# Kernel tuning notes

Measured on AMD Instinct MI355X. Metric: run time of the kernel, lower is better.

## Reference

```python
import jax, jax.numpy as jnp
import numpy as np

L, B, T, D, H, M = 2, 4, 1024, 256, 4, 1024
EPS = 1e-5  # hk.LayerNorm default


def setup_inputs() -> dict:
    key = jax.random.key(0)
    ks = jax.random.split(key, 12)
    s_in = (2.0 / D) ** 0.5       # VarianceScaling(2.0), fan_in = D
    s_o = (2.0 / (H * D)) ** 0.5  # fan_in = H*D for final projection
    s_m = (1.0 / M) ** 0.5
    g = lambda k, shape, s: jax.random.normal(k, shape, jnp.float32) * s
    return {
        "queries": g(ks[0], (B, T, D), 1.0),
        "Wq": g(ks[1], (L, D, H * D), s_in),
        "bq": jnp.zeros((L, H * D), jnp.float32),
        "Wk": g(ks[2], (L, D, H * D), s_in),
        "bk": jnp.zeros((L, H * D), jnp.float32),
        "Wv": g(ks[3], (L, D, H * D), s_in),
        "bv": jnp.zeros((L, H * D), jnp.float32),
        "Wo": g(ks[4], (L, H * D, D), s_o),
        "bo": jnp.zeros((L, D), jnp.float32),
        "ln1_s": jnp.ones((L, D), jnp.float32),
        "ln1_b": jnp.zeros((L, D), jnp.float32),
        "W1": g(ks[5], (L, D, M), s_in),
        "b1": jnp.zeros((L, M), jnp.float32),
        "W2": g(ks[6], (L, M, D), s_m),
        "b2": jnp.zeros((L, D), jnp.float32),
        "ln2_s": jnp.ones((L, D), jnp.float32),
        "ln2_b": jnp.zeros((L, D), jnp.float32),
    }


def _layernorm(x, s, o):
    m = jnp.mean(x, axis=-1, keepdims=True)
    v = jnp.var(x, axis=-1, keepdims=True)
    return (x - m) * jax.lax.rsqrt(v + EPS) * s + o


def _block(x, Wq, bq, Wk, bk, Wv, bv, Wo, bo, ln1_s, ln1_b, W1, b1, W2, b2, ln2_s, ln2_b):
    # Multi-head self-attention with per-head dim = D (key_size == qkv_size)
    q = (x @ Wq + bq).reshape(B, T, H, D)
    k = (x @ Wk + bk).reshape(B, T, H, D)
    v = (x @ Wv + bv).reshape(B, T, H, D)
    q = q / jnp.sqrt(jnp.float32(D))
    attn = jnp.einsum('bqhd,bkhd->bhqk', q, k)   # [B,H,T,T]
    attn = jax.nn.softmax(attn, axis=-1)
    o = jnp.einsum('bhqk,bkhd->bqhd', attn, v).reshape(B, T, H * D)
    o = o @ Wo + bo
    # post-norm residual 1
    x = _layernorm(o + x, ln1_s, ln1_b)
    # MLP: Linear(D->M) + ReLU + Linear(M->D)
    h = jax.nn.relu(x @ W1 + b1)
    m = h @ W2 + b2
    return _layernorm(m + x, ln2_s, ln2_b)


def reference(queries, Wq, bq, Wk, bk, Wv, bv, Wo, bo, ln1_s, ln1_b,
              W1, b1, W2, b2, ln2_s, ln2_b):
    x = queries
    for i in range(L):
        x = _block(x, Wq[i], bq[i], Wk[i], bk[i], Wv[i], bv[i], Wo[i], bo[i],
                   ln1_s[i], ln1_b[i], W1[i], b1[i], W2[i], b2[i],
                   ln2_s[i], ln2_b[i])
    return x
```

## Files before the change

kernel.cpp:

```cpp
#include <hip/hip_runtime.h>
#include <hip/hip_bf16.h>

#define CL 2
#define CB 4
#define CT 1024
#define CD 256
#define CH 4
#define CM 1024
#define CHD (CH * CD)
#define NROW (CB * CT)

typedef unsigned short ushort_t;
typedef __attribute__((ext_vector_type(8))) short short8v;
typedef __attribute__((ext_vector_type(4))) float float4v;

#define LOG2E 1.44269504088896f

__device__ __forceinline__ float bf2f(unsigned short u) {
    return __uint_as_float(((unsigned int)u) << 16);
}
__device__ __forceinline__ unsigned short f2bf(float f) {
    unsigned int x = __float_as_uint(f);
    return (unsigned short)((x + 0x7fffu + ((x >> 16) & 1u)) >> 16);
}

__global__ __launch_bounds__(256) void detect_kernel(
    const ushort_t* __restrict__ w, int n, int* __restrict__ flag)
{
    __shared__ int red[256];
    int c = 0;
    for (int i = threadIdx.x; i < n; i += 256) {
        float v = bf2f(w[i]);
        if (!(fabsf(v) <= 1e6f)) c++;
    }
    red[threadIdx.x] = c;
    __syncthreads();
    for (int s = 128; s > 0; s >>= 1) {
        if (threadIdx.x < s) red[threadIdx.x] += red[threadIdx.x + s];
        __syncthreads();
    }
    if (threadIdx.x == 0) flag[0] = (red[0] < 8) ? 1 : 0;
}

__global__ __launch_bounds__(256) void tconv_all(
    const void* __restrict__ Wq, const void* __restrict__ Wk,
    const void* __restrict__ Wv, const void* __restrict__ W1,
    ushort_t* __restrict__ wqkvT, ushort_t* __restrict__ w1T,
    const int* __restrict__ flagp)
{
    const int fbf = *flagp;
    const int z = blockIdx.z;
    const int which = z >> 1, l = z & 1;
    const void* in = (which == 0) ? Wq : (which == 1) ? Wk
                   : (which == 2) ? Wv : W1;
    ushort_t* out = (which < 3)
        ? wqkvT + (long)l * 3072 * 256 + (long)which * 1024 * 256
        : w1T + (long)l * 1024 * 256;
    const long zi = (long)l * 262144;

    __shared__ float tile[32][33];
    const int r0 = blockIdx.y * 32;
    const int c0 = blockIdx.x * 32;
    const int tx = threadIdx.x & 31;
    const int ty = threadIdx.x >> 5;
#pragma unroll
    for (int i = 0; i < 32; i += 8) {
        const long idx = zi + (long)(r0 + ty + i) * 1024 + c0 + tx;
        tile[ty + i][tx] = fbf ? bf2f(((const ushort_t*)in)[idx])
                               : ((const float*)in)[idx];
    }
    __syncthreads();
#pragma unroll
    for (int i = 0; i < 32; i += 8)
        out[(long)(c0 + ty + i) * 256 + r0 + tx] = f2bf(tile[tx][ty + i]);
}

__global__ __launch_bounds__(256) void tconv2(
    const void* __restrict__ Wo, const void* __restrict__ W2,
    ushort_t* __restrict__ wscr, long ioff, const int* __restrict__ flagp)
{
    const int fbf = *flagp;
    const int z = blockIdx.z;
    const void* in = z ? W2 : Wo;
    ushort_t* out = wscr + (long)z * 262144;

    __shared__ float tile[32][33];
    const int r0 = blockIdx.y * 32;
    const int c0 = blockIdx.x * 32;
    const int tx = threadIdx.x & 31;
    const int ty = threadIdx.x >> 5;
#pragma unroll
    for (int i = 0; i < 32; i += 8) {
        const long idx = ioff + (long)(r0 + ty + i) * 256 + c0 + tx;
        tile[ty + i][tx] = fbf ? bf2f(((const ushort_t*)in)[idx])
                               : ((const float*)in)[idx];
    }
    __syncthreads();
#pragma unroll
    for (int i = 0; i < 32; i += 8)
        out[(long)(c0 + ty + i) * 1024 + r0 + tx] = f2bf(tile[tx][ty + i]);
}

__global__ __launch_bounds__(256) void qkv_proj(
    const ushort_t* __restrict__ A, const ushort_t* __restrict__ B,
    const void* __restrict__ bq, const void* __restrict__ bk,
    const void* __restrict__ bv, ushort_t* __restrict__ qk,
    ushort_t* __restrict__ vT, long boff, const int* __restrict__ flagp)
{
    const long m0 = (long)blockIdx.y * 128;
    const long n0 = (long)blockIdx.x * 128;

    __shared__ __align__(16) ushort_t As[128 * 40];
    __shared__ __align__(16) ushort_t Bs[128 * 40];

    const int tid = threadIdx.x;
    const int wave = tid >> 6;
    const int lane = tid & 63;
    const int quad = lane >> 4;
    const int lrow = lane & 15;
    const int wm = (wave >> 1) * 64;
    const int wn = (wave & 1) * 64;

    float4v acc[4][4];
#pragma unroll
    for (int i = 0; i < 4; ++i)
#pragma unroll
        for (int j = 0; j < 4; ++j)
            acc[i][j] = (float4v){0.f, 0.f, 0.f, 0.f};

    for (int k0 = 0; k0 < 256; k0 += 32) {
        __syncthreads();
#pragma unroll
        for (int p = 0; p < 2; ++p) {
            const int c = p * 256 + tid;
            const int row = c >> 2;
            const int kk = (c & 3) << 3;
            *reinterpret_cast<short8v*>(&As[row * 40 + kk]) =
                *reinterpret_cast<const short8v*>(&A[(m0 + row) * 256 + k0 + kk]);
            *reinterpret_cast<short8v*>(&Bs[row * 40 + kk]) =
                *reinterpret_cast<const short8v*>(&B[(n0 + row) * 256 + k0 + kk]);
        }
        __syncthreads();

        short8v af[4], bfv[4];
#pragma unroll
        for (int i = 0; i < 4; ++i) {
            af[i]  = *reinterpret_cast<const short8v*>(&As[(wm + i * 16 + lrow) * 40 + quad * 8]);
            bfv[i] = *reinterpret_cast<const short8v*>(&Bs[(wn + i * 16 + lrow) * 40 + quad * 8]);
        }
#pragma unroll
        for (int mi = 0; mi < 4; ++mi)
#pragma unroll
            for (int ni = 0; ni < 4; ++ni)
                acc[mi][ni] = __builtin_amdgcn_mfma_f32_16x16x32_bf16(
                    af[mi], bfv[ni], acc[mi][ni], 0, 0, 0);
    }

    const int fbf = *flagp;
#pragma unroll
    for (int mi = 0; mi < 4; ++mi) {
#pragma unroll
        for (int ni = 0; ni < 4; ++ni) {
            const long col = n0 + wn + ni * 16 + lrow;
            const long row0 = m0 + wm + mi * 16 + quad * 4;
            const void* bp;
            long bn;
            if (col < 1024)      { bp = bq; bn = col; }
            else if (col < 2048) { bp = bk; bn = col - 1024; }
            else                 { bp = bv; bn = col - 2048; }
            const float bias = fbf ? bf2f(((const ushort_t*)bp)[boff + bn])
                                   : ((const float*)bp)[boff + bn];
            if (col < 2048) {
#pragma unroll
                for (int r = 0; r < 4; ++r)
                    qk[(row0 + r) * 2048 + col] = f2bf(acc[mi][ni][r] + bias);
            } else {
                const long d = col - 2048;
                const long addr = ((row0 >> 10) << 2) * 262144 + d * 1024 + (row0 & 1023);
                ushort4 u;
                u.x = f2bf(acc[mi][ni][0] + bias);
                u.y = f2bf(acc[mi][ni][1] + bias);
                u.z = f2bf(acc[mi][ni][2] + bias);
                u.w = f2bf(acc[mi][ni][3] + bias);
                *reinterpret_cast<ushort4*>(&vT[addr]) = u;
            }
        }
    }
}

template <int AMODE>
__global__ __launch_bounds__(256) void mgemm64s(
    const ushort_t* __restrict__ A, const ushort_t* __restrict__ Ap1,
    const float2* __restrict__ ml, const ushort_t* __restrict__ B,
    float* __restrict__ P, int K2, int lda, int ldb)
{
    const int z = blockIdx.z;
    const long m0 = (long)blockIdx.y * 64;
    const long n0 = (long)blockIdx.x * 64;
    const int k_beg = z * K2;

    __shared__ __align__(16) ushort_t As[64 * 40];
    __shared__ __align__(16) ushort_t Bs[64 * 40];

    const int tid = threadIdx.x;
    const int wave = tid >> 6;
    const int lane = tid & 63;
    const int quad = lane >> 4;
    const int lrow = lane & 15;
    const int wm = (wave >> 1) * 32;
    const int wn = (wave & 1) * 32;

    const int ar = tid >> 2;
    const int ak = (tid & 3) << 3;

    float4v acc[2][2];
#pragma unroll
    for (int i = 0; i < 2; ++i)
#pragma unroll
        for (int j = 0; j < 2; ++j)
            acc[i][j] = (float4v){0.f, 0.f, 0.f, 0.f};

    for (int k0 = k_beg; k0 < k_beg + K2; k0 += 32) {
        __syncthreads();
        if constexpr (AMODE == 0) {
            *reinterpret_cast<short8v*>(&As[ar * 40 + ak]) =
                *reinterpret_cast<const short8v*>(&A[(m0 + ar) * (long)lda + k0 + ak]);
        } else {
            const long m = m0 + ar;
            const int hh = (k0 + ak) >> 8;
            const int bh = ((int)(m >> 10) << 2) + hh;
            const int trow = (int)(m & 1023);
            const float2 v0 = ml[bh * 1024 + trow];
            const float2 v1 = ml[(16 + bh) * 1024 + trow];
            const float mm = fmaxf(v0.x, v1.x);
            const float a0 = exp2f(v0.x - mm);
            const float a1 = exp2f(v1.x - mm);
            const float inv = 1.0f / (v0.y * a0 + v1.y * a1);
            const ushort4 u0a = *reinterpret_cast<const ushort4*>(&A[m * 1024 + k0 + ak]);
            const ushort4 u0b = *reinterpret_cast<const ushort4*>(&A[m * 1024 + k0 + ak + 4]);
            const ushort4 u1a = *reinterpret_cast<const ushort4*>(&Ap1[m * 1024 + k0 + ak]);
            const ushort4 u1b = *reinterpret_cast<const ushort4*>(&Ap1[m * 1024 + k0 + ak + 4]);
            short8v t8;
            t8[0] = (short)f2bf((bf2f(u0a.x) * a0 + bf2f(u1a.x) * a1) * inv);
            t8[1] = (short)f2bf((bf2f(u0a.y) * a0 + bf2f(u1a.y) * a1) * inv);
            t8[2] = (short)f2bf((bf2f(u0a.z) * a0 + bf2f(u1a.z) * a1) * inv);
            t8[3] = (short)f2bf((bf2f(u0a.w) * a0 + bf2f(u1a.w) * a1) * inv);
            t8[4] = (short)f2bf((bf2f(u0b.x) * a0 + bf2f(u1b.x) * a1) * inv);
            t8[5] = (short)f2bf((bf2f(u0b.y) * a0 + bf2f(u1b.y) * a1) * inv);
            t8[6] = (short)f2bf((bf2f(u0b.z) * a0 + bf2f(u1b.z) * a1) * inv);
            t8[7] = (short)f2bf((bf2f(u0b.w) * a0 + bf2f(u1b.w) * a1) * inv);
            *reinterpret_cast<short8v*>(&As[ar * 40 + ak]) = t8;
        }
        *reinterpret_cast<short8v*>(&Bs[ar * 40 + ak]) =
            *reinterpret_cast<const short8v*>(&B[(n0 + ar) * (long)ldb + k0 + ak]);
        __syncthreads();

        short8v af[2], bfv[2];
#pragma unroll
        for (int i = 0; i < 2; ++i) {
            af[i]  = *reinterpret_cast<const short8v*>(&As[(wm + i * 16 + lrow) * 40 + quad * 8]);
            bfv[i] = *reinterpret_cast<const short8v*>(&Bs[(wn + i * 16 + lrow) * 40 + quad * 8]);
        }
#pragma unroll
        for (int mi = 0; mi < 2; ++mi)
#pragma unroll
            for (int ni = 0; ni < 2; ++ni)
                acc[mi][ni] = __builtin_amdgcn_mfma_f32_16x16x32_bf16(
                    af[mi], bfv[ni], acc[mi][ni], 0, 0, 0);
    }

    float* Pz = P + (long)z * NROW * CD;
#pragma unroll
    for (int mi = 0; mi < 2; ++mi)
#pragma unroll
        for (int ni = 0; ni < 2; ++ni) {
            const long col = n0 + wn + ni * 16 + lrow;
            const long row0 = m0 + wm + mi * 16 + quad * 4;
#pragma unroll
            for (int r = 0; r < 4; ++r)
                Pz[(row0 + r) * CD + col] = acc[mi][ni][r];
        }
}

template <int RELU>
__global__ __launch_bounds__(256) void mgemm64b(
    const ushort_t* __restrict__ A, const ushort_t* __restrict__ B,
    const void* __restrict__ bias, ushort_t* __restrict__ C,
    int K, int lda, int ldb, int ldc, long boff,
    const int* __restrict__ flagp)
{
    const long m0 = (long)blockIdx.y * 64;
    const long n0 = (long)blockIdx.x * 64;

    __shared__ __align__(16) ushort_t As[64 * 40];
    __shared__ __align__(16) ushort_t Bs[64 * 40];

    const int tid = threadIdx.x;
    const int wave = tid >> 6;
    const int lane = tid & 63;
    const int quad = lane >> 4;
    const int lrow = lane & 15;
    const int wm = (wave >> 1) * 32;
    const int wn = (wave & 1) * 32;

    const int ar = tid >> 2;
    const int ak = (tid & 3) << 3;

    float4v acc[2][2];
#pragma unroll
    for (int i = 0; i < 2; ++i)
#pragma unroll
        for (int j = 0; j < 2; ++j)
            acc[i][j] = (float4v){0.f, 0.f, 0.f, 0.f};

    for (int k0 = 0; k0 < K; k0 += 32) {
        __syncthreads();
        *reinterpret_cast<short8v*>(&As[ar * 40 + ak]) =
            *reinterpret_cast<const short8v*>(&A[(m0 + ar) * (long)lda + k0 + ak]);
        *reinterpret_cast<short8v*>(&Bs[ar * 40 + ak]) =
            *reinterpret_cast<const short8v*>(&B[(n0 + ar) * (long)ldb + k0 + ak]);
        __syncthreads();

        short8v af[2], bfv[2];
#pragma unroll
        for (int i = 0; i < 2; ++i) {
            af[i]  = *reinterpret_cast<const short8v*>(&As[(wm + i * 16 + lrow) * 40 + quad * 8]);
            bfv[i] = *reinterpret_cast<const short8v*>(&Bs[(wn + i * 16 + lrow) * 40 + quad * 8]);
        }
#pragma unroll
        for (int mi = 0; mi < 2; ++mi)
#pragma unroll
            for (int ni = 0; ni < 2; ++ni)
                acc[mi][ni] = __builtin_amdgcn_mfma_f32_16x16x32_bf16(
                    af[mi], bfv[ni], acc[mi][ni], 0, 0, 0);
    }

    const int fbf = *flagp;
#pragma unroll
    for (int mi = 0; mi < 2; ++mi)
#pragma unroll
        for (int ni = 0; ni < 2; ++ni) {
            const long col = n0 + wn + ni * 16 + lrow;
            const long row0 = m0 + wm + mi * 16 + quad * 4;
            const float bv = fbf ? bf2f(((const ushort_t*)bias)[boff + col])
                                 : ((const float*)bias)[boff + col];
#pragma unroll
            for (int r = 0; r < 4; ++r) {
                float v = acc[mi][ni][r] + bv;
                if (RELU) v = fmaxf(v, 0.f);
                C[(row0 + r) * (long)ldc + col] = f2bf(v);
            }
        }
}

__global__ __launch_bounds__(256) void flash_attn(
    const ushort_t* __restrict__ qk, const ushort_t* __restrict__ vT,
    ushort_t* __restrict__ op0, ushort_t* __restrict__ op1,
    float2* __restrict__ ml)
{
    const int bx = blockIdx.x;
    const int bh = bx & 15;
    const int qt = (bx >> 4) & 15;
    const int ck = bx >> 8;
    const int b = bh >> 2, h = bh & 3;

    __shared__ __align__(16) ushort_t Ks[32 * 264];
    __shared__ __align__(16) ushort_t Vs[256 * 40];
    __shared__ __align__(16) ushort_t Ps[4][16 * 40];

    const int tid = threadIdx.x;
    const int wave = tid >> 6;
    const int lane = tid & 63;
    const int quad = lane >> 4;
    const int lrow = lane & 15;

    const long qrow0 = (long)b * CT + qt * 64;
    const int qcol = h * 256;
    const int kcol = 1024 + h * 256;
    const long vbase = (long)bh * 256 * 1024;
    const float SC = 0.0625f * LOG2E;

    short8v qf[8];
#pragma unroll
    for (int kk = 0; kk < 8; ++kk)
        qf[kk] = *reinterpret_cast<const short8v*>(
            &qk[(qrow0 + wave * 16 + lrow) * 2048 + qcol + kk * 32 + quad * 8]);

    float mrun = -1e30f, lrun = 0.f;
    float4v oacc[16];
#pragma unroll
    for (int i = 0; i < 16; ++i) oacc[i] = (float4v){0.f, 0.f, 0.f, 0.f};

    const int t_beg = ck * 512;
    for (int t0 = t_beg; t0 < t_beg + 512; t0 += 32) {
        __syncthreads();
#pragma unroll
        for (int p = 0; p < 4; ++p) {
            const int c = p * 256 + tid;
            {
                const int r = c >> 5, col = (c & 31) * 8;
                *reinterpret_cast<short8v*>(&Ks[r * 264 + col]) =
                    *reinterpret_cast<const short8v*>(
                        &qk[((long)b * CT + t0 + r) * 2048 + kcol + col]);
            }
            {
                const int r = c >> 2, col = (c & 3) * 8;
                *reinterpret_cast<short8v*>(&Vs[r * 40 + col]) =
                    *reinterpret_cast<const short8v*>(
                        &vT[vbase + (long)r * 1024 + t0 + col]);
            }
        }
        __syncthreads();

        float4v sacc[2];
        sacc[0] = (float4v){0.f, 0.f, 0.f, 0.f};
        sacc[1] = (float4v){0.f, 0.f, 0.f, 0.f};
#pragma unroll
        for (int kk = 0; kk < 8; ++kk) {
#pragma unroll
            for (int ni = 0; ni < 2; ++ni) {
                short8v bk = *reinterpret_cast<const short8v*>(
                    &Ks[(ni * 16 + lrow) * 264 + kk * 32 + quad * 8]);
                sacc[ni] = __builtin_amdgcn_mfma_f32_16x16x32_bf16(
                    bk, qf[kk], sacc[ni], 0, 0, 0);
            }
        }
#pragma unroll
        for (int ni = 0; ni < 2; ++ni)
#pragma unroll
            for (int r = 0; r < 4; ++r)
                sacc[ni][r] *= SC;

        float mx = fmaxf(fmaxf(fmaxf(sacc[0][0], sacc[0][1]),
                               fmaxf(sacc[0][2], sacc[0][3])),
                         fmaxf(fmaxf(sacc[1][0], sacc[1][1]),
                               fmaxf(sacc[1][2], sacc[1][3])));
        mx = fmaxf(mx, __shfl_xor(mx, 16));
        mx = fmaxf(mx, __shfl_xor(mx, 32));

        if (__ballot(mx > mrun + 1.0f) != 0ull) {
            const float mnew = fmaxf(mrun, mx);
            const float alpha = exp2f(mrun - mnew);
            mrun = mnew;
            lrun *= alpha;
            float a4[4];
#pragma unroll
            for (int r = 0; r < 4; ++r)
                a4[r] = __shfl(alpha, quad * 4 + r);
#pragma unroll
            for (int ni = 0; ni < 16; ++ni)
#pragma unroll
                for (int r = 0; r < 4; ++r)
                    oacc[ni][r] *= a4[r];
        }

        float s = 0.f;
#pragma unroll
        for (int ni = 0; ni < 2; ++ni) {
            ushort4 pu;
#pragma unroll
            for (int r = 0; r < 4; ++r) {
                const float pv = exp2f(sacc[ni][r] - mrun);
                s += pv;
                (&pu.x)[r] = f2bf(pv);
            }
            *reinterpret_cast<ushort4*>(
                &Ps[wave][lrow * 40 + ni * 16 + quad * 4]) = pu;
        }
        s += __shfl_xor(s, 16);
        s += __shfl_xor(s, 32);
        lrun += s;

        {
            short8v ap = *reinterpret_cast<const short8v*>(
                &Ps[wave][lrow * 40 + quad * 8]);
#pragma unroll
            for (int ni = 0; ni < 16; ++ni) {
                short8v bv = *reinterpret_cast<const short8v*>(
                    &Vs[(ni * 16 + lrow) * 40 + quad * 8]);
                oacc[ni] = __builtin_amdgcn_mfma_f32_16x16x32_bf16(
                    ap, bv, oacc[ni], 0, 0, 0);
            }
        }
    }

    if (quad == 0)
        ml[((ck << 4) + bh) * 1024 + qt * 64 + wave * 16 + lrow] =
            make_float2(mrun, lrun);

    ushort_t* op = ck ? op1 : op0;
#pragma unroll
    for (int ni = 0; ni < 16; ++ni)
#pragma unroll
        for (int r = 0; r < 4; ++r)
            op[(qrow0 + wave * 16 + quad * 4 + r) * 1024 + (h << 8) + ni * 16 + lrow]
                = f2bf(oacc[ni][r]);
}

template <int FINAL>
__global__ __launch_bounds__(256) void ln_p(
    const float* __restrict__ p, const void* __restrict__ gb, long gboff,
    const ushort_t* __restrict__ res, const void* __restrict__ sc,
    const void* __restrict__ bi, void* __restrict__ out, long loff,
    const int* __restrict__ flagp)
{
    const int fbf = *flagp;
    const long row = (long)blockIdx.x * CD;
    const int t = threadIdx.x;
    const float gbv = fbf ? bf2f(((const ushort_t*)gb)[gboff + t])
                          : ((const float*)gb)[gboff + t];
    const float x = p[row + t] + p[(long)NROW * CD + row + t] + gbv + bf2f(res[row + t]);

    __shared__ float r1[256];
    __shared__ float r2[256];
    r1[t] = x;
    r2[t] = x * x;
    __syncthreads();
    for (int s = 128; s > 0; s >>= 1) {
        if (t < s) { r1[t] += r1[t + s]; r2[t] += r2[t + s]; }
        __syncthreads();
    }
    const float mean = r1[0] * (1.0f / CD);
    const float var = r2[0] * (1.0f / CD) - mean * mean;
    const float rstd = rsqrtf(var + 1e-5f);
    const float s_v = fbf ? bf2f(((const ushort_t*)sc)[loff + t]) : ((const float*)sc)[loff + t];
    const float b_v = fbf ? bf2f(((const ushort_t*)bi)[loff + t]) : ((const float*)bi)[loff + t];
    const float y = (x - mean) * rstd * s_v + b_v;
    if constexpr (FINAL) {
        if (fbf) ((ushort_t*)out)[row + t] = f2bf(y);
        else     ((float*)out)[row + t] = y;
    } else {
        ((ushort_t*)out)[row + t] = f2bf(y);
    }
}

__global__ __launch_bounds__(256) void in_convert(
    const void* __restrict__ in, ushort_t* __restrict__ x,
    const int* __restrict__ flagp)
{
    const int fbf = *flagp;
    const long i = ((long)blockIdx.x * 256 + threadIdx.x) << 2;
    if (fbf) {
        *reinterpret_cast<ushort4*>(x + i) =
            *reinterpret_cast<const ushort4*>((const ushort_t*)in + i);
    } else {
        float4 f = *reinterpret_cast<const float4*>((const float*)in + i);
        ushort4 u;
        u.x = f2bf(f.x); u.y = f2bf(f.y); u.z = f2bf(f.z); u.w = f2bf(f.w);
        *reinterpret_cast<ushort4*>(x + i) = u;
    }
}

extern "C" void kernel_launch(void* const* d_in, const int* in_sizes, int n_in,
                              void* d_out, int out_size, void* d_ws, size_t ws_size,
                              hipStream_t stream)
{
    const void* queries = d_in[0];
    const void* Wq = d_in[1];  const void* bq = d_in[2];
    const void* Wk = d_in[3];  const void* bk = d_in[4];
    const void* Wv = d_in[5];  const void* bv = d_in[6];
    const void* Wo = d_in[7];  const void* bo = d_in[8];
    const void* ln1s = d_in[9];  const void* ln1b = d_in[10];
    const void* W1 = d_in[11]; const void* b1 = d_in[12];
    const void* W2 = d_in[13]; const void* b2 = d_in[14];
    const void* ln2s = d_in[15]; const void* ln2b = d_in[16];

    char* p = (char*)d_ws;
    int* flagp = (int*)p;             p += 256;
    ushort_t* wqkvT = (ushort_t*)p;   p += (long)CL * 3072 * 256 * 2;
    ushort_t* w1T   = (ushort_t*)p;   p += (long)CL * 1024 * 256 * 2;
    ushort_t* wscr  = (ushort_t*)p;   p += (long)2 * 256 * 1024 * 2;
    ushort_t* xa    = (ushort_t*)p;   p += (long)NROW * CD * 2;
    ushort_t* qk    = (ushort_t*)p;   p += (long)NROW * 2048 * 2;
    ushort_t* vT    = (ushort_t*)p;   p += (long)16 * 256 * 1024 * 2;
    ushort_t* op0   = (ushort_t*)p;   p += (long)NROW * 1024 * 2;
    ushort_t* op1   = (ushort_t*)p;   p += (long)NROW * 1024 * 2;
    float2*   ml    = (float2*)p;     p += (long)2 * 16 * 1024 * 8;
    ushort_t* h     = vT;
    float*    pgem  = (float*)qk;

    detect_kernel<<<1, 256, 0, stream>>>((const ushort_t*)Wq, 2048, flagp);
    tconv_all<<<dim3(32, 8, 8), 256, 0, stream>>>(
        Wq, Wk, Wv, W1, wqkvT, w1T, flagp);
    in_convert<<<(NROW * CD) / 1024, 256, 0, stream>>>(queries, xa, flagp);

    for (int l = 0; l < CL; ++l) {
        qkv_proj<<<dim3(24, 32, 1), 256, 0, stream>>>(
            xa, wqkvT + (long)l * 3072 * 256, bq, bk, bv, qk, vT,
            (long)l * 1024, flagp);
        tconv2<<<dim3(8, 32, 2), 256, 0, stream>>>(
            Wo, W2, wscr, (long)l * 1024 * 256, flagp);
        flash_attn<<<512, 256, 0, stream>>>(qk, vT, op0, op1, ml);
        mgemm64s<1><<<dim3(4, 64, 2), 256, 0, stream>>>(
            op0, op1, ml, wscr, pgem, 512, 1024, 1024);
        ln_p<0><<<NROW, 256, 0, stream>>>(pgem, bo, (long)l * 256, xa,
                                          ln1s, ln1b, xa, (long)l * 256, flagp);
        mgemm64b<1><<<dim3(16, 64, 1), 256, 0, stream>>>(
            xa, w1T + (long)l * 1024 * 256, b1, h,
            256, 256, 256, 1024, (long)l * 1024, flagp);
        mgemm64s<0><<<dim3(4, 64, 2), 256, 0, stream>>>(
            h, nullptr, nullptr, wscr + 262144, pgem, 512, 1024, 1024);
        if (l == CL - 1)
            ln_p<1><<<NROW, 256, 0, stream>>>(pgem, b2, (long)l * 256, xa,
                                              ln2s, ln2b, d_out, (long)l * 256, flagp);
        else
            ln_p<0><<<NROW, 256, 0, stream>>>(pgem, b2, (long)l * 256, xa,
                                              ln2s, ln2b, xa, (long)l * 256, flagp);
    }
}
```

Before: 322.4 us.

## Fuse Wo/W2 transpose into QKV projection launch and deepen GEMM K-tiles

The per-layer weight-transpose kernel is merged into the QKV projection kernel as extra blocks in a flat 1D grid (blocks at index 768 and above do the transpose), which removes one launch per layer. The small 64x64 GEMMs now stage 64-wide K chunks instead of 32, halving the number of barrier pairs per K loop at the cost of more LDS. The split-softmax combine in the attention-output GEMM now computes its per-head rescale factors once, before the K loop, instead of recomputing exp and divide on every iteration. The fused kernel carries the transpose tile in shared memory for every block, which raises LDS use and may lower occupancy.

```diff
diff --git a/kernel.cpp b/kernel.cpp
--- a/kernel.cpp
+++ b/kernel.cpp
@@ -75,45 +75,52 @@
         out[(long)(c0 + ty + i) * 256 + r0 + tx] = f2bf(tile[tx][ty + i]);
 }
 
-__global__ __launch_bounds__(256) void tconv2(
-    const void* __restrict__ Wo, const void* __restrict__ W2,
-    ushort_t* __restrict__ wscr, long ioff, const int* __restrict__ flagp)
-{
-    const int fbf = *flagp;
-    const int z = blockIdx.z;
-    const void* in = z ? W2 : Wo;
-    ushort_t* out = wscr + (long)z * 262144;
-
-    __shared__ float tile[32][33];
-    const int r0 = blockIdx.y * 32;
-    const int c0 = blockIdx.x * 32;
-    const int tx = threadIdx.x & 31;
-    const int ty = threadIdx.x >> 5;
-#pragma unroll
-    for (int i = 0; i < 32; i += 8) {
-        const long idx = ioff + (long)(r0 + ty + i) * 256 + c0 + tx;
-        tile[ty + i][tx] = fbf ? bf2f(((const ushort_t*)in)[idx])
-                               : ((const float*)in)[idx];
-    }
-    __syncthreads();
-#pragma unroll
-    for (int i = 0; i < 32; i += 8)
-        out[(long)(c0 + ty + i) * 1024 + r0 + tx] = f2bf(tile[tx][ty + i]);
-}
-
-__global__ __launch_bounds__(256) void qkv_proj(
+__global__ __launch_bounds__(256) void qkv_tconv(
     const ushort_t* __restrict__ A, const ushort_t* __restrict__ B,
     const void* __restrict__ bq, const void* __restrict__ bk,
     const void* __restrict__ bv, ushort_t* __restrict__ qk,
-    ushort_t* __restrict__ vT, long boff, const int* __restrict__ flagp)
-{
-    const long m0 = (long)blockIdx.y * 128;
-    const long n0 = (long)blockIdx.x * 128;
-
+    ushort_t* __restrict__ vT,
+    const void* __restrict__ Wo, const void* __restrict__ W2,
+    ushort_t* __restrict__ wscr,
+    long boff, long ioff, const int* __restrict__ flagp)
+{
     __shared__ __align__(16) ushort_t As[128 * 40];
     __shared__ __align__(16) ushort_t Bs[128 * 40];
-
+    __shared__ float tile[32][33];
+
+    const int fbf = *flagp;
+    const int bx = blockIdx.x;
     const int tid = threadIdx.x;
+
+    if (bx >= 768) {
+        const int t = bx - 768;
+        const int zx = t & 7;
+        const int zy = (t >> 3) & 31;
+        const int zz = t >> 8;
+        const void* in = zz ? W2 : Wo;
+        ushort_t* out = wscr + (long)zz * 262144;
+        const int r0 = zy * 32;
+        const int c0 = zx * 32;
+        const int tx = tid & 31;
+        const int ty = tid >> 5;
+#pragma unroll
+        for (int i = 0; i < 32; i += 8) {
+            const long idx = ioff + (long)(r0 + ty + i) * 256 + c0 + tx;
+            tile[ty + i][tx] = fbf ? bf2f(((const ushort_t*)in)[idx])
+                                   : ((const float*)in)[idx];
+        }
+        __syncthreads();
+#pragma unroll
+        for (int i = 0; i < 32; i += 8)
+            out[(long)(c0 + ty + i) * 1024 + r0 + tx] = f2bf(tile[tx][ty + i]);
+        return;
+    }
+
+    const int nt = bx % 24;
+    const int mt = bx / 24;
+    const long m0 = (long)mt * 128;
+    const long n0 = (long)nt * 128;
+
     const int wave = tid >> 6;
     const int lane = tid & 63;
     const int quad = lane >> 4;
@@ -156,7 +163,6 @@
                     af[mi], bfv[ni], acc[mi][ni], 0, 0, 0);
     }
 
-    const int fbf = *flagp;
 #pragma unroll
     for (int mi = 0; mi < 4; ++mi) {
 #pragma unroll
@@ -199,8 +205,8 @@
     const long n0 = (long)blockIdx.x * 64;
     const int k_beg = z * K2;
 
-    __shared__ __align__(16) ushort_t As[64 * 40];
-    __shared__ __align__(16) ushort_t Bs[64 * 40];
+    __shared__ __align__(16) ushort_t As[64 * 72];
+    __shared__ __align__(16) ushort_t Bs[64 * 72];
 
     const int tid = threadIdx.x;
     const int wave = tid >> 6;
@@ -213,60 +219,82 @@
     const int ar = tid >> 2;
     const int ak = (tid & 3) << 3;
 
-    float4v acc[2][2];
-#pragma unroll
-    for (int i = 0; i < 2; ++i)
-#pragma unroll
-        for (int j = 0; j < 2; ++j)
-            acc[i][j] = (float4v){0.f, 0.f, 0.f, 0.f};
-
-    for (int k0 = k_beg; k0 < k_beg + K2; k0 += 32) {
-        __syncthreads();
-        if constexpr (AMODE == 0) {
-            *reinterpret_cast<short8v*>(&As[ar * 40 + ak]) =
-                *reinterpret_cast<const short8v*>(&A[(m0 + ar) * (long)lda + k0 + ak]);
-        } else {
-            const long m = m0 + ar;
-            const int hh = (k0 + ak) >> 8;
-            const int bh = ((int)(m >> 10) << 2) + hh;
-            const int trow = (int)(m & 1023);
+    float s0h[2] = {0.f, 0.f}, s1h[2] = {0.f, 0.f};
+    if constexpr (AMODE == 1) {
+        const long m = m0 + ar;
+        const int bhbase = ((int)(m >> 10) << 2);
+        const int trow = (int)(m & 1023);
+        const int h0 = k_beg >> 8;
+#pragma unroll
+        for (int i = 0; i < 2; ++i) {
+            const int bh = bhbase + h0 + i;
             const float2 v0 = ml[bh * 1024 + trow];
             const float2 v1 = ml[(16 + bh) * 1024 + trow];
             const float mm = fmaxf(v0.x, v1.x);
             const float a0 = exp2f(v0.x - mm);
             const float a1 = exp2f(v1.x - mm);
             const float inv = 1.0f / (v0.y * a0 + v1.y * a1);
-            const ushort4 u0a = *reinterpret_cast<const ushort4*>(&A[m * 1024 + k0 + ak]);
-            const ushort4 u0b = *reinterpret_cast<const ushort4*>(&A[m * 1024 + k0 + ak + 4]);
-            const ushort4 u1a = *reinterpret_cast<const ushort4*>(&Ap1[m * 1024 + k0 + ak]);
-            const ushort4 u1b = *reinterpret_cast<const ushort4*>(&Ap1[m * 1024 + k0 + ak + 4]);
-            short8v t8;
-            t8[0] = (short)f2bf((bf2f(u0a.x) * a0 + bf2f(u1a.x) * a1) * inv);
-            t8[1] = (short)f2bf((bf2f(u0a.y) * a0 + bf2f(u1a.y) * a1) * inv);
-            t8[2] = (short)f2bf((bf2f(u0a.z) * a0 + bf2f(u1a.z) * a1) * inv);
-            t8[3] = (short)f2bf((bf2f(u0a.w) * a0 + bf2f(u1a.w) * a1) * inv);
-            t8[4] = (short)f2bf((bf2f(u0b.x) * a0 + bf2f(u1b.x) * a1) * inv);
-            t8[5] = (short)f2bf((bf2f(u0b.y) * a0 + bf2f(u1b.y) * a1) * inv);
-            t8[6] = (short)f2bf((bf2f(u0b.z) * a0 + bf2f(u1b.z) * a1) * inv);
-            t8[7] = (short)f2bf((bf2f(u0b.w) * a0 + bf2f(u1b.w) * a1) * inv);
-            *reinterpret_cast<short8v*>(&As[ar * 40 + ak]) = t8;
-        }
-        *reinterpret_cast<short8v*>(&Bs[ar * 40 + ak]) =
-            *reinterpret_cast<const short8v*>(&B[(n0 + ar) * (long)ldb + k0 + ak]);
-        __syncthreads();
-
-        short8v af[2], bfv[2];
-#pragma unroll
-        for (int i = 0; i < 2; ++i) {
-            af[i]  = *reinterpret_cast<const short8v*>(&As[(wm + i * 16 + lrow) * 40 + quad * 8]);
-            bfv[i] = *reinterpret_cast<const short8v*>(&Bs[(wn + i * 16 + lrow) * 40 + quad * 8]);
-        }
-#pragma unroll
-        for (int mi = 0; mi < 2; ++mi)
-#pragma unroll
-            for (int ni = 0; ni < 2; ++ni)
-                acc[mi][ni] = __builtin_amdgcn_mfma_f32_16x16x32_bf16(
-                    af[mi], bfv[ni], acc[mi][ni], 0, 0, 0);
+            s0h[i] = a0 * inv;
+            s1h[i] = a1 * inv;
+        }
+    }
+
+    float4v acc[2][2];
+#pragma unroll
+    for (int i = 0; i < 2; ++i)
+#pragma unroll
+        for (int j = 0; j < 2; ++j)
+            acc[i][j] = (float4v){0.f, 0.f, 0.f, 0.f};
+
+    for (int k0 = k_beg; k0 < k_beg + K2; k0 += 64) {
+        __syncthreads();
+#pragma unroll
+        for (int p = 0; p < 2; ++p) {
+            const int kc = p * 32 + ak;
+            if constexpr (AMODE == 0) {
+                *reinterpret_cast<short8v*>(&As[ar * 72 + kc]) =
+                    *reinterpret_cast<const short8v*>(&A[(m0 + ar) * (long)lda + k0 + kc]);
+            } else {
+                const long m = m0 + ar;
+                const int hi = ((k0 + kc) >> 8) - (k_beg >> 8);
+                const float s0 = s0h[hi], s1 = s1h[hi];
+                const ushort4 u0a = *reinterpret_cast<const ushort4*>(&A[m * 1024 + k0 + kc]);
+                const ushort4 u0b = *reinterpret_cast<const ushort4*>(&A[m * 1024 + k0 + kc + 4]);
+                const ushort4 u1a = *reinterpret_cast<const ushort4*>(&Ap1[m * 1024 + k0 + kc]);
+                const ushort4 u1b = *reinterpret_cast<const ushort4*>(&Ap1[m * 1024 + k0 + kc + 4]);
+                short8v t8;
+                t8[0] = (short)f2bf(bf2f(u0a.x) * s0 + bf2f(u1a.x) * s1);
+                t8[1] = (short)f2bf(bf2f(u0a.y) * s0 + bf2f(u1a.y) * s1);
+                t8[2] = (short)f2bf(bf2f(u0a.z) * s0 + bf2f(u1a.z) * s1);
+                t8[3] = (short)f2bf(bf2f(u0a.w) * s0 + bf2f(u1a.w) * s1);
+                t8[4] = (short)f2bf(bf2f(u0b.x) * s0 + bf2f(u1b.x) * s1);
+                t8[5] = (short)f2bf(bf2f(u0b.y) * s0 + bf2f(u1b.y) * s1);
+                t8[6] = (short)f2bf(bf2f(u0b.z) * s0 + bf2f(u1b.z) * s1);
+                t8[7] = (short)f2bf(bf2f(u0b.w) * s0 + bf2f(u1b.w) * s1);
+                *reinterpret_cast<short8v*>(&As[ar * 72 + kc]) = t8;
+            }
+            *reinterpret_cast<short8v*>(&Bs[ar * 72 + kc]) =
+                *reinterpret_cast<const short8v*>(&B[(n0 + ar) * (long)ldb + k0 + kc]);
+        }
+        __syncthreads();
+
+#pragma unroll
+        for (int kk = 0; kk < 2; ++kk) {
+            short8v af[2], bfv[2];
+#pragma unroll
+            for (int i = 0; i < 2; ++i) {
+                af[i]  = *reinterpret_cast<const short8v*>(
+                    &As[(wm + i * 16 + lrow) * 72 + kk * 32 + quad * 8]);
+                bfv[i] = *reinterpret_cast<const short8v*>(
+                    &Bs[(wn + i * 16 + lrow) * 72 + kk * 32 + quad * 8]);
+            }
+#pragma unroll
+            for (int mi = 0; mi < 2; ++mi)
+#pragma unroll
+                for (int ni = 0; ni < 2; ++ni)
+                    acc[mi][ni] = __builtin_amdgcn_mfma_f32_16x16x32_bf16(
+                        af[mi], bfv[ni], acc[mi][ni], 0, 0, 0);
+        }
     }
 
     float* Pz = P + (long)z * NROW * CD;
@@ -292,8 +320,8 @@
     const long m0 = (long)blockIdx.y * 64;
     const long n0 = (long)blockIdx.x * 64;
 
-    __shared__ __align__(16) ushort_t As[64 * 40];
-    __shared__ __align__(16) ushort_t Bs[64 * 40];
+    __shared__ __align__(16) ushort_t As[64 * 72];
+    __shared__ __align__(16) ushort_t Bs[64 * 72];
 
     const int tid = threadIdx.x;
     const int wave = tid >> 6;
@@ -313,26 +341,35 @@
         for (int j = 0; j < 2; ++j)
             acc[i][j] = (float4v){0.f, 0.f, 0.f, 0.f};
 
-    for (int k0 = 0; k0 < K; k0 += 32) {
-        __syncthreads();
-        *reinterpret_cast<short8v*>(&As[ar * 40 + ak]) =
-            *reinterpret_cast<const short8v*>(&A[(m0 + ar) * (long)lda + k0 + ak]);
-        *reinterpret_cast<short8v*>(&Bs[ar * 40 + ak]) =
-            *reinterpret_cast<const short8v*>(&B[(n0 + ar) * (long)ldb + k0 + ak]);
-        __syncthreads();
-
-        short8v af[2], bfv[2];
-#pragma unroll
-        for (int i = 0; i < 2; ++i) {
-            af[i]  = *reinterpret_cast<const short8v*>(&As[(wm + i * 16 + lrow) * 40 + quad * 8]);
-            bfv[i] = *reinterpret_cast<const short8v*>(&Bs[(wn + i * 16 + lrow) * 40 + quad * 8]);
-        }
-#pragma unroll
-        for (int mi = 0; mi < 2; ++mi)
-#pragma unroll
-            for (int ni = 0; ni < 2; ++ni)
-                acc[mi][ni] = __builtin_amdgcn_mfma_f32_16x16x32_bf16(
-                    af[mi], bfv[ni], acc[mi][ni], 0, 0, 0);
+    for (int k0 = 0; k0 < K; k0 += 64) {
+        __syncthreads();
+#pragma unroll
+        for (int p = 0; p < 2; ++p) {
+            const int kc = p * 32 + ak;
+            *reinterpret_cast<short8v*>(&As[ar * 72 + kc]) =
+                *reinterpret_cast<const short8v*>(&A[(m0 + ar) * (long)lda + k0 + kc]);
+            *reinterpret_cast<short8v*>(&Bs[ar * 72 + kc]) =
+                *reinterpret_cast<const short8v*>(&B[(n0 + ar) * (long)ldb + k0 + kc]);
+        }
+        __syncthreads();
+
+#pragma unroll
+        for (int kk = 0; kk < 2; ++kk) {
+            short8v af[2], bfv[2];
+#pragma unroll
+            for (int i = 0; i < 2; ++i) {
+                af[i]  = *reinterpret_cast<const short8v*>(
+                    &As[(wm + i * 16 + lrow) * 72 + kk * 32 + quad * 8]);
+                bfv[i] = *reinterpret_cast<const short8v*>(
+                    &Bs[(wn + i * 16 + lrow) * 72 + kk * 32 + quad * 8]);
+            }
+#pragma unroll
+            for (int mi = 0; mi < 2; ++mi)
+#pragma unroll
+                for (int ni = 0; ni < 2; ++ni)
+                    acc[mi][ni] = __builtin_amdgcn_mfma_f32_16x16x32_bf16(
+                        af[mi], bfv[ni], acc[mi][ni], 0, 0, 0);
+        }
     }
 
     const int fbf = *flagp;
@@ -585,11 +622,9 @@
     in_convert<<<(NROW * CD) / 1024, 256, 0, stream>>>(queries, xa, flagp);
 
     for (int l = 0; l < CL; ++l) {
-        qkv_proj<<<dim3(24, 32, 1), 256, 0, stream>>>(
+        qkv_tconv<<<dim3(1280, 1, 1), 256, 0, stream>>>(
             xa, wqkvT + (long)l * 3072 * 256, bq, bk, bv, qk, vT,
-            (long)l * 1024, flagp);
-        tconv2<<<dim3(8, 32, 2), 256, 0, stream>>>(
-            Wo, W2, wscr, (long)l * 1024 * 256, flagp);
+            Wo, W2, wscr, (long)l * 1024, (long)l * 1024 * 256, flagp);
         flash_attn<<<512, 256, 0, stream>>>(qk, vT, op0, op1, ml);
         mgemm64s<1><<<dim3(4, 64, 2), 256, 0, stream>>>(
             op0, op1, ml, wscr, pgem, 512, 1024, 1024);
```

New measurement: 305.2 us. 5.3% less time.
